# Optimization experiments

Hardware: AMD Instinct MI355X
Metric: run time of the kernel (lower is better)

The kernel has to match this reference:

```python
import jax, jax.numpy as jnp
import numpy as np

BIG_Z = 1e6  # sentinel used for background depth when finding the nearest mesh


def setup_inputs() -> dict:
    key = jax.random.key(0)
    ks = jax.random.split(key, 6)
    N, H, W, K = 8, 512, 512, 1      # n_mesh, image H, image W, faces_per_pixel
    F, V, C = 20000, 10002, 32       # faces, verts, feature channels
    zbuf = jax.random.normal(ks[0], (N, H, W, K), jnp.float32)  # ~half negative = background
    pix_to_face = jax.random.randint(ks[1], (N, H, W, K), -1, F)  # -1 = no face
    b = jax.random.uniform(ks[2], (N, H, W, K, 3), jnp.float32) + 1e-3
    bary_coords = b / jnp.sum(b, axis=-1, keepdims=True)
    dists = jax.random.uniform(ks[3], (N, H, W, K), jnp.float32)
    face_memory = jax.random.normal(ks[4], (F, 3, C), jnp.float32)
    packed_faces = jax.random.randint(ks[5], (F, 3), 0, V)
    return {
        "zbuf": zbuf,
        "pix_to_face": pix_to_face,
        "bary_coords": bary_coords,
        "dists": dists,
        "face_memory": face_memory,
        "packed_faces": packed_faces,
        "num_verts": V,
        "mask_duplicate": 0,
    }


def reference(zbuf, pix_to_face, bary_coords, dists, face_memory, packed_faces,
              num_verts, mask_duplicate):
    N = zbuf.shape[0]
    Fn = face_memory.shape[0]

    # per-object mask BEFORE occlusion masking (zbuf[..., 0] >= 0)
    per_obj_mask = zbuf[..., 0] >= 0  # [N,H,W]

    # _mask_occluded_object: pixels covered by >1 mesh
    covered = (zbuf > -1)
    dup = jnp.sum(covered.astype(jnp.float32), axis=0, keepdims=True) > 1  # [1,H,W,K]
    dup = jnp.broadcast_to(dup, zbuf.shape)  # [N,H,W,K]
    if not mask_duplicate:
        # keep the nearest (min-z) mesh at duplicate pixels
        tmp = jnp.where(zbuf < 0, BIG_Z, zbuf)
        min_idx = jnp.argmin(tmp, axis=0)  # [H,W,K]
        mesh_ids = jnp.arange(N).reshape(N, 1, 1, 1)
        dup = dup & (mesh_ids != min_idx[None])

    # mask occluded fragments to -1 (matches in-place boolean writes)
    p = jnp.where(dup, -1, pix_to_face)
    bc = jnp.where(dup[..., None], -1.0, bary_coords)
    d = jnp.where(dup, -1.0, dists)
    zb = jnp.where(dup, -1.0, zbuf)

    # interpolate_face_attributes: gather [N,H,W,K,3,C] then bary-weighted sum,
    # zeroing pixels with pix_to_face < 0
    valid = p >= 0
    safe = jnp.where(valid, p, 0)
    attrs = face_memory[safe]  # [N,H,W,K,3,C]
    out = jnp.einsum('nhwki,nhwkic->nhwkc', bc, attrs)
    out = out * valid[..., None].astype(out.dtype)
    out_map = out[:, :, :, 0, :]               # squeeze K dim -> [N,H,W,C]
    out_map = jnp.transpose(out_map, (0, 3, 1, 2))  # -> [N,C,H,W]

    # vertex visibility: unique visible faces -> their vertices get 1.0
    face_hit = jnp.zeros((Fn,), jnp.float32).at[safe.ravel()].add(
        valid.ravel().astype(jnp.float32))
    face_vis = (face_hit > 0).astype(jnp.float32)  # [F]
    vv = jnp.zeros((num_verts,), jnp.float32).at[packed_faces.ravel()].add(
        jnp.broadcast_to(face_vis[:, None], (Fn, 3)).ravel())
    vertex_visibility_map = (vv > 0).astype(jnp.float32)

    # return out_map, visibility, per-object mask, and masked fragments (frags_clone)
    return out_map, vertex_visibility_map, per_obj_mask, zb, p, d, bc
```

## Files before the change

kernel.cpp:

```cpp
#include <hip/hip_runtime.h>

#define BIG_Z_F 1000000.0f
#define N_MESH 8

typedef float f4 __attribute__((ext_vector_type(4)));
typedef int   i4 __attribute__((ext_vector_type(4)));


__global__ __launch_bounds__(256) void zero_vv(
    float* __restrict__ vv, int V)
{
    const int i = blockIdx.x * blockDim.x + threadIdx.x;
    if (i < V) vv[i] = 0.0f;
}

__global__ __launch_bounds__(256) void raster_fused(
    const f4* __restrict__ zbuf4,
    const i4* __restrict__ p2f4,
    const f4* __restrict__ bary4,
    const f4* __restrict__ dists4,
    const float* __restrict__ fmem,
    const int* __restrict__ pfaces,
    const int* __restrict__ mdp,
    f4* __restrict__ out_map4,
    f4* __restrict__ maskO4,
    f4* __restrict__ zbO4,
    f4* __restrict__ pO4,
    f4* __restrict__ dO4,
    f4* __restrict__ bcO4,
    float* __restrict__ vv,
    int HW4, int C)
{
    const int q = blockIdx.x * blockDim.x + threadIdx.x;
    if (q >= HW4) return;
    const int n    = blockIdx.y;
    const int idx4 = n * HW4 + q;
    const int md   = *mdp;

    int   cnt[4]  = { 0, 0, 0, 0 };
    float best[4] = { __builtin_inff(), __builtin_inff(),
                      __builtin_inff(), __builtin_inff() };
    int   bi[4]   = { 0, 0, 0, 0 };
    f4 zown;
    #pragma unroll
    for (int nn = 0; nn < N_MESH; ++nn) {
        const f4 v = zbuf4[nn * HW4 + q];
        if (nn == n) zown = v;
        #pragma unroll
        for (int j = 0; j < 4; ++j) {
            const float zv = v[j];
            cnt[j] += (zv > -1.0f) ? 1 : 0;
            const float t = (zv < 0.0f) ? BIG_Z_F : zv;
            if (t < best[j]) { best[j] = t; bi[j] = nn; }
        }
    }

    bool dup[4];
    {
        f4 m, zb;
        #pragma unroll
        for (int j = 0; j < 4; ++j) {
            const bool dup0 = (cnt[j] > 1);
            dup[j] = dup0 && ((md != 0) || (n != bi[j]));
            m[j]  = (zown[j] >= 0.0f) ? 1.0f : 0.0f;
            zb[j] = dup[j] ? -1.0f : zown[j];
        }
        __builtin_nontemporal_store(m,  &maskO4[idx4]);
        __builtin_nontemporal_store(zb, &zbO4[idx4]);
    }

    const i4 praw = __builtin_nontemporal_load(&p2f4[idx4]);
    const f4 drw  = __builtin_nontemporal_load(&dists4[idx4]);
    const f4 bv0  = __builtin_nontemporal_load(&bary4[idx4 * 3 + 0]);
    const f4 bv1  = __builtin_nontemporal_load(&bary4[idx4 * 3 + 1]);
    const f4 bv2  = __builtin_nontemporal_load(&bary4[idx4 * 3 + 2]);
    const int   pr[4] = { praw.x, praw.y, praw.z, praw.w };
    const float dr[4] = { drw.x, drw.y, drw.z, drw.w };
    const float br[4][3] = {
        { bv0.x, bv0.y, bv0.z },
        { bv0.w, bv1.x, bv1.y },
        { bv1.z, bv1.w, bv2.x },
        { bv2.y, bv2.z, bv2.w },
    };

    float bst[4][3];
    float bc[4][3];
    int   safe[4];
    bool  vld[4];
    f4 pOv, dOv;
    #pragma unroll
    for (int j = 0; j < 4; ++j) {
        const int  p     = dup[j] ? -1 : pr[j];
        const bool valid = (p >= 0);
        #pragma unroll
        for (int k = 0; k < 3; ++k) {
            bst[j][k] = dup[j] ? -1.0f : br[j][k];
            bc[j][k]  = valid ? bst[j][k] : 0.0f;
        }
        safe[j] = valid ? p : 0;
        vld[j]  = valid;
        pOv[j]  = (float)p;
        dOv[j]  = dup[j] ? -1.0f : dr[j];
    }
    __builtin_nontemporal_store(pOv, &pO4[idx4]);
    __builtin_nontemporal_store(dOv, &dO4[idx4]);
    {
        f4 c0, c1, c2;
        c0.x = bst[0][0]; c0.y = bst[0][1]; c0.z = bst[0][2]; c0.w = bst[1][0];
        c1.x = bst[1][1]; c1.y = bst[1][2]; c1.z = bst[2][0]; c1.w = bst[2][1];
        c2.x = bst[2][2]; c2.y = bst[3][0]; c2.z = bst[3][1]; c2.w = bst[3][2];
        __builtin_nontemporal_store(c0, &bcO4[idx4 * 3 + 0]);
        __builtin_nontemporal_store(c1, &bcO4[idx4 * 3 + 1]);
        __builtin_nontemporal_store(c2, &bcO4[idx4 * 3 + 2]);
    }

    #pragma unroll
    for (int j = 0; j < 4; ++j) {
        if (vld[j]) {
            const int b = safe[j] * 3;
            vv[pfaces[b + 0]] = 1.0f;
            vv[pfaces[b + 1]] = 1.0f;
            vv[pfaces[b + 2]] = 1.0f;
        }
    }

    const float* ab[4];
    #pragma unroll
    for (int j = 0; j < 4; ++j)
        ab[j] = fmem + (size_t)safe[j] * 3 * C;

    #pragma unroll
    for (int c4 = 0; c4 < 32; c4 += 4) {
        f4 r[4];
        #pragma unroll
        for (int j = 0; j < 4; ++j) {
            const float* a = ab[j];
            const f4 a0 = *(const f4*)(a + c4);
            const f4 a1 = *(const f4*)(a + C + c4);
            const f4 a2 = *(const f4*)(a + 2 * C + c4);
            r[j] = bc[j][0] * a0 + bc[j][1] * a1 + bc[j][2] * a2;
        }
        #pragma unroll
        for (int k = 0; k < 4; ++k) {
            f4 o;
            o.x = r[0][k]; o.y = r[1][k]; o.z = r[2][k]; o.w = r[3][k];
            __builtin_nontemporal_store(o, &out_map4[(size_t)(n * C + c4 + k) * HW4 + q]);
        }
    }
}

extern "C" void kernel_launch(void* const* d_in, const int* in_sizes, int n_in,
                              void* d_out, int out_size, void* d_ws, size_t ws_size,
                              hipStream_t stream) {
    const float* zbuf   = (const float*)d_in[0];
    const int*   p2f    = (const int*)  d_in[1];
    const float* bary   = (const float*)d_in[2];
    const float* dists  = (const float*)d_in[3];
    const float* fmem   = (const float*)d_in[4];
    const int*   pfaces = (const int*)  d_in[5];
    const int*   mdp    = (const int*)  d_in[7];

    const long long P  = in_sizes[0];
    const int HW  = (int)(P / N_MESH);
    const int HW4 = HW / 4;
    const int F3  = in_sizes[5];
    const int C   = in_sizes[4] / F3;
    const int V   = (int)((long long)out_size - P * C - 7 * P);

    float* out     = (float*)d_out;
    float* out_map = out;
    float* vv      = out_map + P * C;
    float* maskO   = vv + V;
    float* zbO     = maskO + P;
    float* pO      = zbO + P;
    float* dO      = pO + P;
    float* bcO     = dO + P;

    zero_vv<<<dim3((V + 255) / 256), dim3(256), 0, stream>>>(vv, V);

    raster_fused<<<dim3(HW4 / 256, N_MESH), dim3(256), 0, stream>>>(
        (const f4*)zbuf, (const i4*)p2f, (const f4*)bary, (const f4*)dists,
        fmem, pfaces, mdp,
        (f4*)out_map, (f4*)maskO, (f4*)zbO, (f4*)pO, (f4*)dO, (f4*)bcO,
        vv, HW4, C);
}
```

Measured before the change: 395.4 us.

## Process one pixel per thread instead of four with scalar accesses

Switches the fused kernel from four pixels per thread with float4 loads and stores to one pixel per thread with scalar loads and stores, launching four times as many threads. The goal is to cut register pressure and raise occupancy so more independent face-memory gathers are in flight, and the gather is reordered so each vertex row is read in sequence. In exchange, per-pixel output stores shrink from 16-byte vectors to 4-byte scalars, and the strided bary loads and stores become less efficient.

```diff
diff --git a/kernel.cpp b/kernel.cpp
--- a/kernel.cpp
+++ b/kernel.cpp
@@ -4,7 +4,6 @@
 #define N_MESH 8
 
 typedef float f4 __attribute__((ext_vector_type(4)));
-typedef int   i4 __attribute__((ext_vector_type(4)));
 
 
 __global__ __launch_bounds__(256) void zero_vv(
@@ -15,136 +14,99 @@
 }
 
 __global__ __launch_bounds__(256) void raster_fused(
-    const f4* __restrict__ zbuf4,
-    const i4* __restrict__ p2f4,
-    const f4* __restrict__ bary4,
-    const f4* __restrict__ dists4,
+    const float* __restrict__ zbuf,
+    const int*   __restrict__ p2f,
+    const float* __restrict__ bary,
+    const float* __restrict__ dists,
     const float* __restrict__ fmem,
-    const int* __restrict__ pfaces,
-    const int* __restrict__ mdp,
-    f4* __restrict__ out_map4,
-    f4* __restrict__ maskO4,
-    f4* __restrict__ zbO4,
-    f4* __restrict__ pO4,
-    f4* __restrict__ dO4,
-    f4* __restrict__ bcO4,
+    const int*   __restrict__ pfaces,
+    const int*   __restrict__ mdp,
+    float* __restrict__ out_map,
+    float* __restrict__ maskO,
+    float* __restrict__ zbO,
+    float* __restrict__ pO,
+    float* __restrict__ dO,
+    float* __restrict__ bcO,
     float* __restrict__ vv,
-    int HW4, int C)
+    int HW, int C)
 {
-    const int q = blockIdx.x * blockDim.x + threadIdx.x;
-    if (q >= HW4) return;
-    const int n    = blockIdx.y;
-    const int idx4 = n * HW4 + q;
-    const int md   = *mdp;
+    const int pix = blockIdx.x * blockDim.x + threadIdx.x;
+    if (pix >= HW) return;
+    const int n   = blockIdx.y;
+    const int idx = n * HW + pix;
+    const int md  = *mdp;
 
-    int   cnt[4]  = { 0, 0, 0, 0 };
-    float best[4] = { __builtin_inff(), __builtin_inff(),
-                      __builtin_inff(), __builtin_inff() };
-    int   bi[4]   = { 0, 0, 0, 0 };
-    f4 zown;
+    int   cnt  = 0;
+    float best = __builtin_inff();
+    int   bi   = 0;
+    float zown = 0.0f;
     #pragma unroll
     for (int nn = 0; nn < N_MESH; ++nn) {
-        const f4 v = zbuf4[nn * HW4 + q];
-        if (nn == n) zown = v;
-        #pragma unroll
-        for (int j = 0; j < 4; ++j) {
-            const float zv = v[j];
-            cnt[j] += (zv > -1.0f) ? 1 : 0;
-            const float t = (zv < 0.0f) ? BIG_Z_F : zv;
-            if (t < best[j]) { best[j] = t; bi[j] = nn; }
-        }
+        const float zv = zbuf[nn * HW + pix];
+        if (nn == n) zown = zv;
+        cnt += (zv > -1.0f) ? 1 : 0;
+        const float t = (zv < 0.0f) ? BIG_Z_F : zv;
+        if (t < best) { best = t; bi = nn; }
+    }
+    const bool dup = (cnt > 1) && ((md != 0) || (n != bi));
+
+    __builtin_nontemporal_store((zown >= 0.0f) ? 1.0f : 0.0f, &maskO[idx]);
+    __builtin_nontemporal_store(dup ? -1.0f : zown, &zbO[idx]);
+
+    const int   praw = __builtin_nontemporal_load(&p2f[idx]);
+    const float drw  = __builtin_nontemporal_load(&dists[idx]);
+    const float br0  = bary[idx * 3 + 0];
+    const float br1  = bary[idx * 3 + 1];
+    const float br2  = bary[idx * 3 + 2];
+
+    const int  p     = dup ? -1 : praw;
+    const bool valid = (p >= 0);
+    const int  safe  = valid ? p : 0;
+
+    const float bst0 = dup ? -1.0f : br0;
+    const float bst1 = dup ? -1.0f : br1;
+    const float bst2 = dup ? -1.0f : br2;
+    const float bc0  = valid ? bst0 : 0.0f;
+    const float bc1  = valid ? bst1 : 0.0f;
+    const float bc2  = valid ? bst2 : 0.0f;
+
+    __builtin_nontemporal_store((float)p, &pO[idx]);
+    __builtin_nontemporal_store(dup ? -1.0f : drw, &dO[idx]);
+    __builtin_nontemporal_store(bst0, &bcO[idx * 3 + 0]);
+    __builtin_nontemporal_store(bst1, &bcO[idx * 3 + 1]);
+    __builtin_nontemporal_store(bst2, &bcO[idx * 3 + 2]);
+
+    if (valid) {
+        const int b = safe * 3;
+        vv[pfaces[b + 0]] = 1.0f;
+        vv[pfaces[b + 1]] = 1.0f;
+        vv[pfaces[b + 2]] = 1.0f;
     }
 
-    bool dup[4];
-    {
-        f4 m, zb;
-        #pragma unroll
-        for (int j = 0; j < 4; ++j) {
-            const bool dup0 = (cnt[j] > 1);
-            dup[j] = dup0 && ((md != 0) || (n != bi[j]));
-            m[j]  = (zown[j] >= 0.0f) ? 1.0f : 0.0f;
-            zb[j] = dup[j] ? -1.0f : zown[j];
-        }
-        __builtin_nontemporal_store(m,  &maskO4[idx4]);
-        __builtin_nontemporal_store(zb, &zbO4[idx4]);
+    const float* a = fmem + (size_t)safe * 3 * C;
+    f4 acc[8];
+    #pragma unroll
+    for (int c4 = 0; c4 < 8; ++c4) {
+        const f4 a0 = *(const f4*)(a + 4 * c4);
+        acc[c4] = bc0 * a0;
     }
-
-    const i4 praw = __builtin_nontemporal_load(&p2f4[idx4]);
-    const f4 drw  = __builtin_nontemporal_load(&dists4[idx4]);
-    const f4 bv0  = __builtin_nontemporal_load(&bary4[idx4 * 3 + 0]);
-    const f4 bv1  = __builtin_nontemporal_load(&bary4[idx4 * 3 + 1]);
-    const f4 bv2  = __builtin_nontemporal_load(&bary4[idx4 * 3 + 2]);
-    const int   pr[4] = { praw.x, praw.y, praw.z, praw.w };
-    const float dr[4] = { drw.x, drw.y, drw.z, drw.w };
-    const float br[4][3] = {
-        { bv0.x, bv0.y, bv0.z },
-        { bv0.w, bv1.x, bv1.y },
-        { bv1.z, bv1.w, bv2.x },
-        { bv2.y, bv2.z, bv2.w },
-    };
-
-    float bst[4][3];
-    float bc[4][3];
-    int   safe[4];
-    bool  vld[4];
-    f4 pOv, dOv;
     #pragma unroll
-    for (int j = 0; j < 4; ++j) {
-        const int  p     = dup[j] ? -1 : pr[j];
-        const bool valid = (p >= 0);
-        #pragma unroll
-        for (int k = 0; k < 3; ++k) {
-            bst[j][k] = dup[j] ? -1.0f : br[j][k];
-            bc[j][k]  = valid ? bst[j][k] : 0.0f;
-        }
-        safe[j] = valid ? p : 0;
-        vld[j]  = valid;
-        pOv[j]  = (float)p;
-        dOv[j]  = dup[j] ? -1.0f : dr[j];
+    for (int c4 = 0; c4 < 8; ++c4) {
+        const f4 a1 = *(const f4*)(a + C + 4 * c4);
+        acc[c4] += bc1 * a1;
     }
-    __builtin_nontemporal_store(pOv, &pO4[idx4]);
-    __builtin_nontemporal_store(dOv, &dO4[idx4]);
-    {
-        f4 c0, c1, c2;
-        c0.x = bst[0][0]; c0.y = bst[0][1]; c0.z = bst[0][2]; c0.w = bst[1][0];
-        c1.x = bst[1][1]; c1.y = bst[1][2]; c1.z = bst[2][0]; c1.w = bst[2][1];
-        c2.x = bst[2][2]; c2.y = bst[3][0]; c2.z = bst[3][1]; c2.w = bst[3][2];
-        __builtin_nontemporal_store(c0, &bcO4[idx4 * 3 + 0]);
-        __builtin_nontemporal_store(c1, &bcO4[idx4 * 3 + 1]);
-        __builtin_nontemporal_store(c2, &bcO4[idx4 * 3 + 2]);
+    #pragma unroll
+    for (int c4 = 0; c4 < 8; ++c4) {
+        const f4 a2 = *(const f4*)(a + 2 * C + 4 * c4);
+        acc[c4] += bc2 * a2;
     }
 
     #pragma unroll
-    for (int j = 0; j < 4; ++j) {
-        if (vld[j]) {
-            const int b = safe[j] * 3;
-            vv[pfaces[b + 0]] = 1.0f;
-            vv[pfaces[b + 1]] = 1.0f;
-            vv[pfaces[b + 2]] = 1.0f;
-        }
-    }
-
-    const float* ab[4];
-    #pragma unroll
-    for (int j = 0; j < 4; ++j)
-        ab[j] = fmem + (size_t)safe[j] * 3 * C;
-
-    #pragma unroll
-    for (int c4 = 0; c4 < 32; c4 += 4) {
-        f4 r[4];
-        #pragma unroll
-        for (int j = 0; j < 4; ++j) {
-            const float* a = ab[j];
-            const f4 a0 = *(const f4*)(a + c4);
-            const f4 a1 = *(const f4*)(a + C + c4);
-            const f4 a2 = *(const f4*)(a + 2 * C + c4);
-            r[j] = bc[j][0] * a0 + bc[j][1] * a1 + bc[j][2] * a2;
-        }
+    for (int c4 = 0; c4 < 8; ++c4) {
         #pragma unroll
         for (int k = 0; k < 4; ++k) {
-            f4 o;
-            o.x = r[0][k]; o.y = r[1][k]; o.z = r[2][k]; o.w = r[3][k];
-            __builtin_nontemporal_store(o, &out_map4[(size_t)(n * C + c4 + k) * HW4 + q]);
+            __builtin_nontemporal_store(
+                acc[c4][k], &out_map[(size_t)(n * C + c4 * 4 + k) * HW + pix]);
         }
     }
 }
@@ -162,7 +124,6 @@
 
     const long long P  = in_sizes[0];
     const int HW  = (int)(P / N_MESH);
-    const int HW4 = HW / 4;
     const int F3  = in_sizes[5];
     const int C   = in_sizes[4] / F3;
     const int V   = (int)((long long)out_size - P * C - 7 * P);
@@ -178,9 +139,8 @@
 
     zero_vv<<<dim3((V + 255) / 256), dim3(256), 0, stream>>>(vv, V);
 
-    raster_fused<<<dim3(HW4 / 256, N_MESH), dim3(256), 0, stream>>>(
-        (const f4*)zbuf, (const i4*)p2f, (const f4*)bary, (const f4*)dists,
-        fmem, pfaces, mdp,
-        (f4*)out_map, (f4*)maskO, (f4*)zbO, (f4*)pO, (f4*)dO, (f4*)bcO,
-        vv, HW4, C);
+    raster_fused<<<dim3(HW / 256, N_MESH), dim3(256), 0, stream>>>(
+        zbuf, p2f, bary, dists, fmem, pfaces, mdp,
+        out_map, maskO, zbO, pO, dO, bcO,
+        vv, HW, C);
 }
```

New measurement: 405.2 us. +2.5%, slower.
